# Kernel tuning notes

Measured on AMD Instinct MI355X. Metric: run time of the kernel, lower is better.

The kernel has to match this reference:

```python
import jax, jax.numpy as jnp
import numpy as np

B, C, H, W = 8, 512, 64, 64
IC = C // 2  # inter_channel


def setup_inputs() -> dict:
    key = jax.random.key(0)
    ks = jax.random.split(key, 10)
    s = 0.02
    return {
        "x": jax.random.normal(ks[0], (B, C, H, W), dtype=jnp.float32),
        "y": jax.random.normal(ks[1], (B, C, H, W), dtype=jnp.float32),
        "w_phi": jax.random.normal(ks[2], (IC, C), dtype=jnp.float32) * s,
        "b_phi": jnp.zeros((IC,), dtype=jnp.float32),
        "w_theta": jax.random.normal(ks[3], (IC, C), dtype=jnp.float32) * s,
        "b_theta": jnp.zeros((IC,), dtype=jnp.float32),
        "w_g": jax.random.normal(ks[4], (IC, C), dtype=jnp.float32) * s,
        "b_g": jnp.zeros((IC,), dtype=jnp.float32),
        "w_mask": jax.random.normal(ks[5], (C, IC), dtype=jnp.float32) * s,
        "b_mask": jnp.zeros((C,), dtype=jnp.float32),
    }


def _conv1x1(w, b, t):
    # t: [b, cin, h, w]; 1x1 conv == channel matmul
    return jnp.einsum('oc,bchw->bohw', w, t) + b[None, :, None, None]


def reference(x, y, w_phi, b_phi, w_theta, b_theta, w_g, b_g, w_mask, b_mask):
    b, c, h, w = x.shape
    ic = w_phi.shape[0]  # c // 2
    # Faithful to the torch code: conv outputs ic channels but is viewed as
    # (b, c, -1), so the sequence length is N = h*w//2 and feature dim is c.
    x_phi = _conv1x1(w_phi, b_phi, y).reshape(b, c, -1)              # [b, c, N]
    x_theta = _conv1x1(w_theta, b_theta, x).reshape(b, c, -1)
    x_theta = jnp.transpose(x_theta, (0, 2, 1))                      # [b, N, c]
    x_g = _conv1x1(w_g, b_g, x).reshape(b, c, -1)
    dict
    x_g = jnp.transpose(x_g, (0, 2, 1))                              # [b, N, c]
    scores = jnp.einsum('bnc,bcm->bnm', x_theta, x_phi)              # [b, N, N]
    attn = jax.nn.softmax(scores, axis=1)  # softmax over dim=1 (columns), as in torch
    out_nl = jnp.einsum('bnm,bmc->bnc', attn, x_g)                   # [b, N, c]
    out_nl = jnp.transpose(out_nl, (0, 2, 1)).reshape(b, ic, h, w)   # [b, ic, h, w]
    mask = _conv1x1(w_mask, b_mask, out_nl)                          # [b, c, h, w]
    return mask + x
```

## Files before the change

kernel.cpp:

```cpp
#include <hip/hip_runtime.h>
#include <hip/hip_bf16.h>


typedef __attribute__((ext_vector_type(8))) short short8;
typedef __attribute__((ext_vector_type(4))) short short4v;
typedef __attribute__((ext_vector_type(4))) float f32x4;

enum { EPI_BF16 = 0, EPI_BF16_BIAS = 1 };

__device__ __forceinline__ short f2bf(float f) {
  union { __hip_bfloat16 h; short s; } u; u.h = __float2bfloat16(f); return u.s;
}
__device__ __forceinline__ float bf2f(short s) {
  union { short s; __hip_bfloat16 h; } u; u.s = s; return __bfloat162float(u.h);
}

__device__ __forceinline__ void async_ld16(const void* g, void* l) {
  __builtin_amdgcn_global_load_lds(
      (const __attribute__((address_space(1))) unsigned int*)(unsigned long long)g,
      (__attribute__((address_space(3))) unsigned int*)(unsigned int)(unsigned long long)l,
      16, 0, 0);
}

template<int EPI>
__global__ __launch_bounds__(512, 4)
void gemm8(const short* __restrict__ Ag, long sA, int lda,
           const short* __restrict__ Bg, long sB, int ldb,
           short* __restrict__ Cg, long sC, int ldc,
           int K, const float* __restrict__ bias)
{
  __shared__ __align__(16) short As[128 * 32];
  __shared__ __align__(16) short Bs[128 * 32];
  const int bz = blockIdx.z;
  const short* A = Ag + (long)bz * sA;
  const short* B = Bg + (long)bz * sB;
  const int m0 = blockIdx.y * 128;
  const int n0 = blockIdx.x * 128;
  const int t = threadIdx.x;
  const int wv = t >> 6, ln = t & 63;
  const int wr = wv >> 1, wc = wv & 1;
  const int fr = ln & 15, q8 = (ln >> 4) * 8;
  const int rowA = t >> 2, kc = (t & 3) * 8;

  f32x4 acc[2][4];
  #pragma unroll
  for (int i = 0; i < 2; i++)
    #pragma unroll
    for (int j = 0; j < 4; j++)
      #pragma unroll
      for (int r = 0; r < 4; r++) acc[i][j][r] = 0.f;

  for (int kk = 0; kk < K; kk += 32) {
    async_ld16(A + (long)(m0 + rowA) * lda + kk + kc, As + wv * 512);
    async_ld16(B + (long)(n0 + rowA) * ldb + kk + kc, Bs + wv * 512);
    __syncthreads();
    short8 af[2], bfr[4];
    #pragma unroll
    for (int mi = 0; mi < 2; mi++) af[mi] = *(const short8*)&As[(wr * 32 + mi * 16 + fr) * 32 + q8];
    #pragma unroll
    for (int ni = 0; ni < 4; ni++) bfr[ni] = *(const short8*)&Bs[(wc * 64 + ni * 16 + fr) * 32 + q8];
    #pragma unroll
    for (int mi = 0; mi < 2; mi++)
      #pragma unroll
      for (int ni = 0; ni < 4; ni++)
        acc[mi][ni] = __builtin_amdgcn_mfma_f32_16x16x32_bf16(af[mi], bfr[ni], acc[mi][ni], 0, 0, 0);
    __syncthreads();
  }

  const int colb = n0 + wc * 64 + fr;
  const int rowb = m0 + wr * 32 + (ln >> 4) * 4;
  #pragma unroll
  for (int mi = 0; mi < 2; mi++)
    #pragma unroll
    for (int r = 0; r < 4; r++) {
      const int mr = rowb + mi * 16 + r;
      float badd = 0.f;
      if constexpr (EPI == EPI_BF16_BIAS) badd = bias[mr];
      #pragma unroll
      for (int ni = 0; ni < 4; ni++)
        Cg[(long)bz * sC + (long)mr * ldc + colb + ni * 16] = f2bf(acc[mi][ni][r] + badd);
    }
}

__global__ __launch_bounds__(512, 4)
void ov_k(const short* __restrict__ Eg, const short* __restrict__ Gg,
          short* __restrict__ Cg)
{
  const int L = blockIdx.x;
  const int xcd = L & 7, k = L >> 3;
  const int slab = xcd + ((k >> 2) << 3);
  const int bz = slab >> 4, by = slab & 15, bx = k & 3;

  __shared__ __align__(16) short As[128 * 32];
  __shared__ __align__(16) short Bs[128 * 32];
  const short* A = Eg + ((long)bz << 22);
  const short* B = Gg + ((long)bz << 20);
  const int m0 = by * 128;
  const int n0 = bx * 128;
  const int t = threadIdx.x;
  const int wv = t >> 6, ln = t & 63;
  const int wr = wv >> 1, wc = wv & 1;
  const int fr = ln & 15, q8 = (ln >> 4) * 8;
  const int rowA = t >> 2, kc = (t & 3) * 8;

  f32x4 acc[2][4];
  #pragma unroll
  for (int i = 0; i < 2; i++)
    #pragma unroll
    for (int j = 0; j < 4; j++)
      #pragma unroll
      for (int r = 0; r < 4; r++) acc[i][j][r] = 0.f;

  for (int kk = 0; kk < 2048; kk += 32) {
    async_ld16(A + (long)(m0 + rowA) * 2048 + kk + kc, As + wv * 512);
    async_ld16(B + (long)(n0 + rowA) * 2048 + kk + kc, Bs + wv * 512);
    __syncthreads();
    short8 af[2], bfr[4];
    #pragma unroll
    for (int mi = 0; mi < 2; mi++) af[mi] = *(const short8*)&As[(wr * 32 + mi * 16 + fr) * 32 + q8];
    #pragma unroll
    for (int ni = 0; ni < 4; ni++) bfr[ni] = *(const short8*)&Bs[(wc * 64 + ni * 16 + fr) * 32 + q8];
    #pragma unroll
    for (int mi = 0; mi < 2; mi++)
      #pragma unroll
      for (int ni = 0; ni < 4; ni++)
        acc[mi][ni] = __builtin_amdgcn_mfma_f32_16x16x32_bf16(af[mi], bfr[ni], acc[mi][ni], 0, 0, 0);
    __syncthreads();
  }

  const int colb = n0 + wc * 64 + fr;
  const int rowb = m0 + wr * 32 + (ln >> 4) * 4;
  #pragma unroll
  for (int mi = 0; mi < 2; mi++)
    #pragma unroll
    for (int r = 0; r < 4; r++) {
      const int mr = rowb + mi * 16 + r;
      #pragma unroll
      for (int ni = 0; ni < 4; ni++)
        Cg[((long)bz << 20) + (long)mr * 512 + colb + ni * 16] = f2bf(acc[mi][ni][r]);
    }
}

__global__ __launch_bounds__(256)
void conv_pt(const short* __restrict__ imgT,
             const short* __restrict__ wth, const short* __restrict__ wph,
             const float* __restrict__ bth, const float* __restrict__ bph,
             short* __restrict__ TPT2)
{
  __shared__ __align__(16) short As[128 * 32];
  __shared__ __align__(16) short Bs[128 * 32];
  const int m0 = blockIdx.y * 128;
  const int n0 = blockIdx.x * 128;
  const bool isphi = blockIdx.y >= 256;
  const short* A = imgT + (long)m0 * 512;
  const short* B = isphi ? wph : wth;
  const float* bias = isphi ? bph : bth;
  const int t = threadIdx.x;
  const int wv = t >> 6, ln = t & 63;
  const int wm = (wv >> 1) * 64, wn = (wv & 1) * 64;
  const int fr = ln & 15, q8 = (ln >> 4) * 8;
  const int rowA = t >> 2, kc = (t & 3) * 8;

  f32x4 acc[4][4];
  #pragma unroll
  for (int i = 0; i < 4; i++)
    #pragma unroll
    for (int j = 0; j < 4; j++)
      #pragma unroll
      for (int r = 0; r < 4; r++) acc[i][j][r] = 0.f;

  for (int kk = 0; kk < 512; kk += 32) {
    #pragma unroll
    for (int s = 0; s < 2; s++) {
      async_ld16(A + (long)(s * 64 + rowA) * 512 + kk + kc, As + (s * 256 + wv * 64) * 8);
      async_ld16(B + (long)(n0 + s * 64 + rowA) * 512 + kk + kc, Bs + (s * 256 + wv * 64) * 8);
    }
    __syncthreads();
    short8 af[4], bfr[4];
    #pragma unroll
    for (int mi = 0; mi < 4; mi++) af[mi] = *(const short8*)&As[(wm + mi * 16 + fr) * 32 + q8];
    #pragma unroll
    for (int ni = 0; ni < 4; ni++) bfr[ni] = *(const short8*)&Bs[(wn + ni * 16 + fr) * 32 + q8];
    #pragma unroll
    for (int mi = 0; mi < 4; mi++)
      #pragma unroll
      for (int ni = 0; ni < 4; ni++)
        acc[mi][ni] = __builtin_amdgcn_mfma_f32_16x16x32_bf16(af[mi], bfr[ni], acc[mi][ni], 0, 0, 0);
    __syncthreads();
  }

  const int colb = n0 + wn + fr;
  const int rowb = m0 + wm + (ln >> 4) * 4;
  float cb[4];
  #pragma unroll
  for (int ni = 0; ni < 4; ni++) cb[ni] = bias[colb + ni * 16];
  #pragma unroll
  for (int mi = 0; mi < 4; mi++)
    #pragma unroll
    for (int r = 0; r < 4; r++) {
      const long mr = rowb + mi * 16 + r;
      #pragma unroll
      for (int ni = 0; ni < 4; ni++)
        TPT2[mr * 256 + colb + ni * 16] = f2bf(acc[mi][ni][r] + cb[ni]);
    }
}

__global__ __launch_bounds__(256)
void scores_k(const short* __restrict__ TT2, const short* __restrict__ PT2,
              short* __restrict__ ST, float* __restrict__ pstats)
{
  __shared__ __align__(16) short As[128 * 32];
  __shared__ __align__(16) short Bs[128 * 32];
  const int bz = blockIdx.z, by = blockIdx.y, bx = blockIdx.x;
  const int t = threadIdx.x;
  const int wv = t >> 6, ln = t & 63;
  const int wm = (wv >> 1) * 64, wn = (wv & 1) * 64;
  const int fr = ln & 15, q8 = (ln >> 4) * 8;
  const int rowA = t >> 2, kc = (t & 3) * 8;

  f32x4 acc[4][4];
  #pragma unroll
  for (int i = 0; i < 4; i++)
    #pragma unroll
    for (int j = 0; j < 4; j++)
      #pragma unroll
      for (int r = 0; r < 4; r++) acc[i][j][r] = 0.f;

  #pragma unroll
  for (int h = 0; h < 2; h++) {
    const short* Aseg = TT2 + ((long)(bz * 4096 + h * 2048 + by * 128)) * 256;
    const short* Bseg = PT2 + ((long)(bz * 4096 + h * 2048 + bx * 128)) * 256;
    for (int kk = 0; kk < 256; kk += 32) {
      #pragma unroll
      for (int s = 0; s < 2; s++) {
        async_ld16(Aseg + (long)(s * 64 + rowA) * 256 + kk + kc, As + (s * 256 + wv * 64) * 8);
        async_ld16(Bseg + (long)(s * 64 + rowA) * 256 + kk + kc, Bs + (s * 256 + wv * 64) * 8);
      }
      __syncthreads();
      short8 af[4], bfr[4];
      #pragma unroll
      for (int mi = 0; mi < 4; mi++) af[mi] = *(const short8*)&As[(wm + mi * 16 + fr) * 32 + q8];
      #pragma unroll
      for (int ni = 0; ni < 4; ni++) bfr[ni] = *(const short8*)&Bs[(wn + ni * 16 + fr) * 32 + q8];
      #pragma unroll
      for (int mi = 0; mi < 4; mi++)
        #pragma unroll
        for (int ni = 0; ni < 4; ni++)
          acc[mi][ni] = __builtin_amdgcn_mfma_f32_16x16x32_bf16(af[mi], bfr[ni], acc[mi][ni], 0, 0, 0);
      __syncthreads();
    }
  }

  const int colb = bx * 128 + wn + fr;
  const int rowb = by * 128 + wm + (ln >> 4) * 4;
  short* base = ST + ((long)bz << 22);
  float ps[4] = {0.f, 0.f, 0.f, 0.f};
  #pragma unroll
  for (int mi = 0; mi < 4; mi++)
    #pragma unroll
    for (int r = 0; r < 4; r++) {
      const long mr = rowb + mi * 16 + r;
      #pragma unroll
      for (int ni = 0; ni < 4; ni++) {
        float e = __expf(acc[mi][ni][r]);
        base[mr * 2048 + colb + ni * 16] = f2bf(e);
        ps[ni] += e;
      }
    }
  #pragma unroll
  for (int ni = 0; ni < 4; ni++) {
    ps[ni] += __shfl_xor(ps[ni], 16);
    ps[ni] += __shfl_xor(ps[ni], 32);
  }
  float* part = (float*)As;
  if (ln < 16) {
    #pragma unroll
    for (int ni = 0; ni < 4; ni++)
      part[(wv >> 1) * 128 + wn + ni * 16 + fr] = ps[ni];
  }
  __syncthreads();
  if (t < 128)
    pstats[((long)(bz * 16 + by)) * 2048 + bx * 128 + t] = part[t] + part[128 + t];
}

__global__ __launch_bounds__(256)
void zfinal(const float* __restrict__ pstats, float* __restrict__ invZ)
{
  const int g = blockIdx.x * 256 + threadIdx.x;
  const int b = g >> 11, col = g & 2047;
  float S = 0.f;
  #pragma unroll
  for (int rc = 0; rc < 16; rc++) S += pstats[((long)(b * 16 + rc)) * 2048 + col];
  invZ[g] = 1.f / S;
}

__global__ __launch_bounds__(256)
void g_scale(short* __restrict__ G, const float* __restrict__ invZ)
{
  const long base = ((long)blockIdx.x * 256 + threadIdx.x) * 8;
  const int bz = (int)(base >> 20);
  const int n2 = (int)(base & 4095);
  const float* z = invZ + bz * 2048 + (n2 & 2047);
  short8 v = *(short8*)&G[base];
  f32x4 z0 = *(const f32x4*)z;
  f32x4 z1 = *(const f32x4*)(z + 4);
  #pragma unroll
  for (int j = 0; j < 4; j++) { v[j] = f2bf(bf2f(v[j]) * z0[j]); v[4 + j] = f2bf(bf2f(v[4 + j]) * z1[j]); }
  *(short8*)&G[base] = v;
}

__global__ __launch_bounds__(256)
void mask_k(const short* __restrict__ Wm20, const short* __restrict__ Wm21,
            const short* __restrict__ OVT, const float* __restrict__ bmask,
            const float* __restrict__ x, float* __restrict__ out)
{
  __shared__ __align__(16) short As[128 * 32];
  __shared__ __align__(16) short Bs[128 * 32];
  const int bz = blockIdx.z;
  const int n0 = blockIdx.x * 128;
  const int m0 = blockIdx.y * 128;
  const short* A = (n0 >= 2048) ? Wm21 : Wm20;
  const short* B = OVT + ((long)bz << 20) + (long)(n0 & 2047) * 512;
  const int t = threadIdx.x;
  const int wv = t >> 6, ln = t & 63;
  const int wm = (wv >> 1) * 64, wn = (wv & 1) * 64;
  const int fr = ln & 15, q8 = (ln >> 4) * 8;
  const int rowA = t >> 2, kc = (t & 3) * 8;

  f32x4 acc[4][4];
  #pragma unroll
  for (int i = 0; i < 4; i++)
    #pragma unroll
    for (int j = 0; j < 4; j++)
      #pragma unroll
      for (int r = 0; r < 4; r++) acc[i][j][r] = 0.f;

  for (int kk = 0; kk < 512; kk += 32) {
    #pragma unroll
    for (int s = 0; s < 2; s++) {
      async_ld16(A + (long)(m0 + s * 64 + rowA) * 512 + kk + kc, As + (s * 256 + wv * 64) * 8);
      async_ld16(B + (long)(s * 64 + rowA) * 512 + kk + kc, Bs + (s * 256 + wv * 64) * 8);
    }
    __syncthreads();
    short8 af[4], bfr[4];
    #pragma unroll
    for (int mi = 0; mi < 4; mi++) af[mi] = *(const short8*)&As[(wm + mi * 16 + fr) * 32 + q8];
    #pragma unroll
    for (int ni = 0; ni < 4; ni++) bfr[ni] = *(const short8*)&Bs[(wn + ni * 16 + fr) * 32 + q8];
    #pragma unroll
    for (int mi = 0; mi < 4; mi++)
      #pragma unroll
      for (int ni = 0; ni < 4; ni++)
        acc[mi][ni] = __builtin_amdgcn_mfma_f32_16x16x32_bf16(af[mi], bfr[ni], acc[mi][ni], 0, 0, 0);
    __syncthreads();
  }

  const int colb = n0 + wn + fr;
  const int rowb = m0 + wm + (ln >> 4) * 4;
  #pragma unroll
  for (int mi = 0; mi < 4; mi++)
    #pragma unroll
    for (int r = 0; r < 4; r++) {
      const int mr = rowb + mi * 16 + r;
      const float badd = bmask[mr];
      const long rbase = ((long)bz * 512 + mr) * 4096;
      #pragma unroll
      for (int ni = 0; ni < 4; ni++) {
        const int cc = colb + ni * 16;
        out[rbase + cc] = acc[mi][ni][r] + badd + x[rbase + cc];
      }
    }
}

__global__ __launch_bounds__(256)
void wconv2(const float* w_phi, const float* w_theta, const float* w_g,
            const float* w_mask,
            short* wph, short* wth, short* wg, short* Wm20, short* Wm21)
{
  const int seg = blockIdx.x >> 6;
  const int blk = blockIdx.x & 63;
  const int i0 = blk * 2048 + threadIdx.x * 8;
  if (seg < 3) {
    const float* s = seg == 0 ? w_phi : seg == 1 ? w_theta : w_g;
    short* d = seg == 0 ? wph : seg == 1 ? wth : wg;
    f32x4 a = *(const f32x4*)&s[i0];
    f32x4 b = *(const f32x4*)&s[i0 + 4];
    short8 o;
    #pragma unroll
    for (int j = 0; j < 4; j++) { o[j] = f2bf(a[j]); o[4 + j] = f2bf(b[j]); }
    *(short8*)&d[i0] = o;
  } else {
    const int o = i0 >> 8;
    f32x4 a = *(const f32x4*)&w_mask[i0];
    f32x4 b = *(const f32x4*)&w_mask[i0 + 4];
    short v[8];
    #pragma unroll
    for (int j = 0; j < 4; j++) { v[j] = f2bf(a[j]); v[4 + j] = f2bf(b[j]); }
    short8 a0, a1, b0, b1;
    #pragma unroll
    for (int j = 0; j < 4; j++) {
      a0[2 * j] = v[j];     a0[2 * j + 1] = 0;
      a1[2 * j] = v[4 + j]; a1[2 * j + 1] = 0;
      b0[2 * j] = 0;        b0[2 * j + 1] = v[j];
      b1[2 * j] = 0;        b1[2 * j + 1] = v[4 + j];
    }
    const long base = (long)o * 512 + 2 * (i0 & 255);
    *(short8*)&Wm20[base] = a0; *(short8*)&Wm20[base + 8] = a1;
    *(short8*)&Wm21[base] = b0; *(short8*)&Wm21[base + 8] = b1;
  }
}

__global__ __launch_bounds__(256)
void convtr(const float* __restrict__ x, const float* __restrict__ y,
            short* __restrict__ xT, short* __restrict__ yT)
{
  __shared__ __align__(16) short Ts[64 * 136];
  const int z = blockIdx.z;
  const float* src = (z < 8 ? x : y) + (long)(z & 7) * 512 * 4096;
  short* dst = (z < 8 ? xT : yT) + (long)(z & 7) * 4096 * 512;
  const int c0 = blockIdx.y * 128;
  const int n0 = blockIdx.x * 64;
  const int t = threadIdx.x;

  const int i16 = t & 15;
  const int rbase = t >> 4;
  const int sw = (i16 & 3) << 3;
  f32x4 v[8];
  #pragma unroll
  for (int p = 0; p < 8; p++)
    v[p] = *(const f32x4*)&src[(long)(c0 + p * 16 + rbase) * 4096 + n0 + i16 * 4];
  #pragma unroll
  for (int p = 0; p < 8; p++) {
    const int c = p * 16 + rbase;
    const int cs = c ^ sw;
    #pragma unroll
    for (int j = 0; j < 4; j++)
      Ts[(i16 * 4 + j) * 136 + cs] = f2bf(v[p][j]);
  }
  __syncthreads();

  #pragma unroll
  for (int q = 0; q < 4; q++) {
    const int idx = q * 256 + t;
    const int px = idx >> 4;
    const int p16 = idx & 15;
    const int sw2 = ((px >> 2) & 3) << 3;
    short8 o = *(const short8*)&Ts[px * 136 + ((p16 * 8) ^ sw2)];
    *(short8*)&dst[(long)(n0 + px) * 512 + c0 + p16 * 8] = o;
  }
}

extern "C" void kernel_launch(void* const* d_in, const int* in_sizes, int n_in,
                              void* d_out, int out_size, void* d_ws, size_t ws_size,
                              hipStream_t stream)
{
  (void)in_sizes; (void)n_in; (void)out_size; (void)ws_size;
  const float* x       = (const float*)d_in[0];
  const float* y       = (const float*)d_in[1];
  const float* w_phi   = (const float*)d_in[2];
  const float* b_phi   = (const float*)d_in[3];
  const float* w_theta = (const float*)d_in[4];
  const float* b_theta = (const float*)d_in[5];
  const float* w_g     = (const float*)d_in[6];
  const float* b_g     = (const float*)d_in[7];
  const float* w_mask  = (const float*)d_in[8];
  const float* b_mask  = (const float*)d_in[9];
  float* out = (float*)d_out;

  char* ws = (char*)d_ws;
  const long MB = 1L << 20;
  short* wph  = (short*)(ws + 0);
  short* wth  = (short*)(ws + 256 * 1024);
  short* wg   = (short*)(ws + 512 * 1024);
  short* Wm20 = (short*)(ws + 768 * 1024);
  short* Wm21 = (short*)(ws + 1280 * 1024);
  short* xT   = (short*)(ws + 2 * MB);
  short* yT   = (short*)(ws + 34 * MB);
  short* TPT2 = (short*)(ws + 66 * MB);
  short* G    = (short*)(ws + 98 * MB);
  short* ST   = (short*)(ws + 2 * MB);
  float* pstats = (float*)(ws + 114 * MB);
  float* invZ   = (float*)(ws + 115 * MB);
  short* OVT  = (short*)(ws + 66 * MB);

  dim3 blk(256, 1, 1);
  dim3 blk8(512, 1, 1);

  wconv2<<<dim3(256, 1, 1), blk, 0, stream>>>(w_phi, w_theta, w_g, w_mask,
                                              wph, wth, wg, Wm20, Wm21);
  convtr<<<dim3(64, 4, 16), blk, 0, stream>>>(x, y, xT, yT);

  conv_pt<<<dim3(2, 512, 1), blk, 0, stream>>>(xT, wth, wph, b_theta, b_phi, TPT2);

  gemm8<EPI_BF16_BIAS><<<dim3(32, 2, 8), blk8, 0, stream>>>(
      wg, 0, 512, xT, 4096L * 512, 512, G, 1048576L, 4096, 512, b_g);

  scores_k<<<dim3(16, 16, 8), blk, 0, stream>>>(TPT2, TPT2 + 32768L * 256, ST, pstats);
  zfinal<<<dim3(64, 1, 1), blk, 0, stream>>>(pstats, invZ);
  g_scale<<<dim3(4096, 1, 1), blk, 0, stream>>>(G, invZ);

  ov_k<<<dim3(512, 1, 1), blk8, 0, stream>>>(ST, G, OVT);

  mask_k<<<dim3(32, 4, 8), blk, 0, stream>>>(Wm20, Wm21, OVT, b_mask, x, out);
}
```

Baseline: 393.3 us.

## Halve mask GEMM K, remap scores tiles per XCD, batch convtr tiles

Mask GEMM drops the zero-interleaved doubled weight matrices and instead uses the compact 256-wide weight with a column offset into OVT, halving its K loop and weight traffic. Scores kernel remaps a flat block index so neighbouring 4x4 tile groups land on the same XCD for L2 reuse. Convtr processes four 64-pixel chunks per block with the next loads issued before the stores, overlapping memory work. The ov_k B-operand addressing also changes to a strided layout. Several unrelated changes carry mixed risk.

```diff
diff --git a/kernel.cpp b/kernel.cpp
--- a/kernel.cpp
+++ b/kernel.cpp
@@ -103,6 +103,9 @@
   const int fr = ln & 15, q8 = (ln >> 4) * 8;
   const int rowA = t >> 2, kc = (t & 3) * 8;
 
+  const int jB = n0 + rowA;
+  const long boff = (long)(jB & 255) * 4096 + (long)(jB >> 8) * 2048;
+
   f32x4 acc[2][4];
   #pragma unroll
   for (int i = 0; i < 2; i++)
@@ -113,7 +116,7 @@
 
   for (int kk = 0; kk < 2048; kk += 32) {
     async_ld16(A + (long)(m0 + rowA) * 2048 + kk + kc, As + wv * 512);
-    async_ld16(B + (long)(n0 + rowA) * 2048 + kk + kc, Bs + wv * 512);
+    async_ld16(B + boff + kk + kc, Bs + wv * 512);
     __syncthreads();
     short8 af[2], bfr[4];
     #pragma unroll
@@ -211,7 +214,13 @@
 {
   __shared__ __align__(16) short As[128 * 32];
   __shared__ __align__(16) short Bs[128 * 32];
-  const int bz = blockIdx.z, by = blockIdx.y, bx = blockIdx.x;
+  const int L = blockIdx.x;
+  const int xcd = L & 7, s = L >> 3;
+  const int st = xcd + 8 * (s >> 4);
+  const int inner = s & 15;
+  const int by = (st >> 2) * 4 + (inner >> 2);
+  const int bx = (st & 3) * 4 + (inner & 3);
+  const int bz = blockIdx.z;
   const int t = threadIdx.x;
   const int wv = t >> 6, ln = t & 63;
   const int wm = (wv >> 1) * 64, wn = (wv & 1) * 64;
@@ -232,9 +241,9 @@
     const short* Bseg = PT2 + ((long)(bz * 4096 + h * 2048 + bx * 128)) * 256;
     for (int kk = 0; kk < 256; kk += 32) {
       #pragma unroll
-      for (int s = 0; s < 2; s++) {
-        async_ld16(Aseg + (long)(s * 64 + rowA) * 256 + kk + kc, As + (s * 256 + wv * 64) * 8);
-        async_ld16(Bseg + (long)(s * 64 + rowA) * 256 + kk + kc, Bs + (s * 256 + wv * 64) * 8);
+      for (int s2 = 0; s2 < 2; s2++) {
+        async_ld16(Aseg + (long)(s2 * 64 + rowA) * 256 + kk + kc, As + (s2 * 256 + wv * 64) * 8);
+        async_ld16(Bseg + (long)(s2 * 64 + rowA) * 256 + kk + kc, Bs + (s2 * 256 + wv * 64) * 8);
       }
       __syncthreads();
       short8 af[4], bfr[4];
@@ -310,17 +319,17 @@
 }
 
 __global__ __launch_bounds__(256)
-void mask_k(const short* __restrict__ Wm20, const short* __restrict__ Wm21,
-            const short* __restrict__ OVT, const float* __restrict__ bmask,
-            const float* __restrict__ x, float* __restrict__ out)
+void mask_k(const short* __restrict__ Wm, const short* __restrict__ OVT,
+            const float* __restrict__ bmask, const float* __restrict__ x,
+            float* __restrict__ out)
 {
   __shared__ __align__(16) short As[128 * 32];
   __shared__ __align__(16) short Bs[128 * 32];
   const int bz = blockIdx.z;
   const int n0 = blockIdx.x * 128;
   const int m0 = blockIdx.y * 128;
-  const short* A = (n0 >= 2048) ? Wm21 : Wm20;
-  const short* B = OVT + ((long)bz << 20) + (long)(n0 & 2047) * 512;
+  const short* B = OVT + ((long)bz << 20) + (long)(n0 & 2047) * 512
+                   + ((n0 >= 2048) ? 256 : 0);
   const int t = threadIdx.x;
   const int wv = t >> 6, ln = t & 63;
   const int wm = (wv >> 1) * 64, wn = (wv & 1) * 64;
@@ -335,10 +344,10 @@
       #pragma unroll
       for (int r = 0; r < 4; r++) acc[i][j][r] = 0.f;
 
-  for (int kk = 0; kk < 512; kk += 32) {
+  for (int kk = 0; kk < 256; kk += 32) {
     #pragma unroll
     for (int s = 0; s < 2; s++) {
-      async_ld16(A + (long)(m0 + s * 64 + rowA) * 512 + kk + kc, As + (s * 256 + wv * 64) * 8);
+      async_ld16(Wm + (long)(m0 + s * 64 + rowA) * 256 + kk + kc, As + (s * 256 + wv * 64) * 8);
       async_ld16(B + (long)(s * 64 + rowA) * 512 + kk + kc, Bs + (s * 256 + wv * 64) * 8);
     }
     __syncthreads();
@@ -375,39 +384,19 @@
 __global__ __launch_bounds__(256)
 void wconv2(const float* w_phi, const float* w_theta, const float* w_g,
             const float* w_mask,
-            short* wph, short* wth, short* wg, short* Wm20, short* Wm21)
+            short* wph, short* wth, short* wg, short* wm)
 {
   const int seg = blockIdx.x >> 6;
   const int blk = blockIdx.x & 63;
   const int i0 = blk * 2048 + threadIdx.x * 8;
-  if (seg < 3) {
-    const float* s = seg == 0 ? w_phi : seg == 1 ? w_theta : w_g;
-    short* d = seg == 0 ? wph : seg == 1 ? wth : wg;
-    f32x4 a = *(const f32x4*)&s[i0];
-    f32x4 b = *(const f32x4*)&s[i0 + 4];
-    short8 o;
-    #pragma unroll
-    for (int j = 0; j < 4; j++) { o[j] = f2bf(a[j]); o[4 + j] = f2bf(b[j]); }
-    *(short8*)&d[i0] = o;
-  } else {
-    const int o = i0 >> 8;
-    f32x4 a = *(const f32x4*)&w_mask[i0];
-    f32x4 b = *(const f32x4*)&w_mask[i0 + 4];
-    short v[8];
-    #pragma unroll
-    for (int j = 0; j < 4; j++) { v[j] = f2bf(a[j]); v[4 + j] = f2bf(b[j]); }
-    short8 a0, a1, b0, b1;
-    #pragma unroll
-    for (int j = 0; j < 4; j++) {
-      a0[2 * j] = v[j];     a0[2 * j + 1] = 0;
-      a1[2 * j] = v[4 + j]; a1[2 * j + 1] = 0;
-      b0[2 * j] = 0;        b0[2 * j + 1] = v[j];
-      b1[2 * j] = 0;        b1[2 * j + 1] = v[4 + j];
-    }
-    const long base = (long)o * 512 + 2 * (i0 & 255);
-    *(short8*)&Wm20[base] = a0; *(short8*)&Wm20[base + 8] = a1;
-    *(short8*)&Wm21[base] = b0; *(short8*)&Wm21[base + 8] = b1;
-  }
+  const float* s = seg == 0 ? w_phi : seg == 1 ? w_theta : seg == 2 ? w_g : w_mask;
+  short* d = seg == 0 ? wph : seg == 1 ? wth : seg == 2 ? wg : wm;
+  f32x4 a = *(const f32x4*)&s[i0];
+  f32x4 b = *(const f32x4*)&s[i0 + 4];
+  short8 o;
+  #pragma unroll
+  for (int j = 0; j < 4; j++) { o[j] = f2bf(a[j]); o[4 + j] = f2bf(b[j]); }
+  *(short8*)&d[i0] = o;
 }
 
 __global__ __launch_bounds__(256)
@@ -419,34 +408,42 @@
   const float* src = (z < 8 ? x : y) + (long)(z & 7) * 512 * 4096;
   short* dst = (z < 8 ? xT : yT) + (long)(z & 7) * 4096 * 512;
   const int c0 = blockIdx.y * 128;
-  const int n0 = blockIdx.x * 64;
+  const int nb = blockIdx.x * 256;
   const int t = threadIdx.x;
-
   const int i16 = t & 15;
   const int rbase = t >> 4;
   const int sw = (i16 & 3) << 3;
+
   f32x4 v[8];
   #pragma unroll
   for (int p = 0; p < 8; p++)
-    v[p] = *(const f32x4*)&src[(long)(c0 + p * 16 + rbase) * 4096 + n0 + i16 * 4];
-  #pragma unroll
-  for (int p = 0; p < 8; p++) {
-    const int c = p * 16 + rbase;
-    const int cs = c ^ sw;
-    #pragma unroll
-    for (int j = 0; j < 4; j++)
-      Ts[(i16 * 4 + j) * 136 + cs] = f2bf(v[p][j]);
-  }
-  __syncthreads();
-
-  #pragma unroll
-  for (int q = 0; q < 4; q++) {
-    const int idx = q * 256 + t;
-    const int px = idx >> 4;
-    const int p16 = idx & 15;
-    const int sw2 = ((px >> 2) & 3) << 3;
-    short8 o = *(const short8*)&Ts[px * 136 + ((p16 * 8) ^ sw2)];
-    *(short8*)&dst[(long)(n0 + px) * 512 + c0 + p16 * 8] = o;
+    v[p] = *(const f32x4*)&src[(long)(c0 + p * 16 + rbase) * 4096 + nb + i16 * 4];
+
+  for (int it = 0; it < 4; it++) {
+    const int n0 = nb + it * 64;
+    __syncthreads();
+    #pragma unroll
+    for (int p = 0; p < 8; p++) {
+      const int cs = (p * 16 + rbase) ^ sw;
+      #pragma unroll
+      for (int j = 0; j < 4; j++)
+        Ts[(i16 * 4 + j) * 136 + cs] = f2bf(v[p][j]);
+    }
+    __syncthreads();
+    if (it < 3) {
+      #pragma unroll
+      for (int p = 0; p < 8; p++)
+        v[p] = *(const f32x4*)&src[(long)(c0 + p * 16 + rbase) * 4096 + (n0 + 64) + i16 * 4];
+    }
+    #pragma unroll
+    for (int q = 0; q < 4; q++) {
+      const int idx = q * 256 + t;
+      const int px = idx >> 4;
+      const int p16 = idx & 15;
+      const int sw2 = ((px >> 2) & 3) << 3;
+      short8 o = *(const short8*)&Ts[px * 136 + ((p16 * 8) ^ sw2)];
+      *(short8*)&dst[(long)(n0 + px) * 512 + c0 + p16 * 8] = o;
+    }
   }
 }
 
@@ -472,8 +469,7 @@
   short* wph  = (short*)(ws + 0);
   short* wth  = (short*)(ws + 256 * 1024);
   short* wg   = (short*)(ws + 512 * 1024);
-  short* Wm20 = (short*)(ws + 768 * 1024);
-  short* Wm21 = (short*)(ws + 1280 * 1024);
+  short* wm   = (short*)(ws + 768 * 1024);
   short* xT   = (short*)(ws + 2 * MB);
   short* yT   = (short*)(ws + 34 * MB);
   short* TPT2 = (short*)(ws + 66 * MB);
@@ -487,19 +483,19 @@
   dim3 blk8(512, 1, 1);
 
   wconv2<<<dim3(256, 1, 1), blk, 0, stream>>>(w_phi, w_theta, w_g, w_mask,
-                                              wph, wth, wg, Wm20, Wm21);
-  convtr<<<dim3(64, 4, 16), blk, 0, stream>>>(x, y, xT, yT);
+                                              wph, wth, wg, wm);
+  convtr<<<dim3(16, 4, 16), blk, 0, stream>>>(x, y, xT, yT);
 
   conv_pt<<<dim3(2, 512, 1), blk, 0, stream>>>(xT, wth, wph, b_theta, b_phi, TPT2);
 
   gemm8<EPI_BF16_BIAS><<<dim3(32, 2, 8), blk8, 0, stream>>>(
       wg, 0, 512, xT, 4096L * 512, 512, G, 1048576L, 4096, 512, b_g);
 
-  scores_k<<<dim3(16, 16, 8), blk, 0, stream>>>(TPT2, TPT2 + 32768L * 256, ST, pstats);
+  scores_k<<<dim3(256, 1, 8), blk, 0, stream>>>(TPT2, TPT2 + 32768L * 256, ST, pstats);
   zfinal<<<dim3(64, 1, 1), blk, 0, stream>>>(pstats, invZ);
   g_scale<<<dim3(4096, 1, 1), blk, 0, stream>>>(G, invZ);
 
   ov_k<<<dim3(512, 1, 1), blk8, 0, stream>>>(ST, G, OVT);
 
-  mask_k<<<dim3(32, 4, 8), blk, 0, stream>>>(Wm20, Wm21, OVT, b_mask, x, out);
-}
+  mask_k<<<dim3(32, 4, 8), blk, 0, stream>>>(wm, OVT, b_mask, x, out);
+}
```

Result: slower. 422.8 us (+7.5%).
